# Performance work log

Hardware: AMD Instinct MI355X
Metric: run time of the kernel (lower is better)

The kernel has to match this reference:

```python
import jax, jax.numpy as jnp
import numpy as np
from jax.scipy.special import gammaln

REG = 1e-6
NHLOG2PI = -0.5 * float(np.log(2.0 * np.pi))


def _log_besseli(s, kappa):
    # Uniform asymptotic expansion (leading order) of log I_s(kappa):
    # I_s(s*x) ~ exp(s*eta) / (sqrt(2*pi*s) * (1+x^2)^(1/4))
    x = kappa / s
    sq = jnp.sqrt(1.0 + x * x)
    eta = sq + jnp.log(x) - jnp.log1p(sq)
    return s * eta - 0.5 * jnp.log(2.0 * jnp.pi * s) - 0.5 * jnp.log(sq)


def _log_C_vmf(d, kappa):
    # log C_d(kappa) = d*(-0.5 log 2pi) + s*log(kappa) - log I_s(kappa), s = d/2 - 1
    s = 0.5 * d - 1.0
    return d * NHLOG2PI + s * jnp.log(kappa) - _log_besseli(s, kappa)


def _log_surface_area(dim):
    # HypersphericalUniform.__log_surface_area
    h = (dim + 1.0) / 2.0
    return np.log(2.0) + h * np.log(np.pi) - float(jax.scipy.special.gammaln(jnp.asarray(h, jnp.float32)))


def _vmf_layer(x, w_mu, w_logk, b_mu, b_logk, in_f, out_f):
    # eval mode: weight = mu (unit-normalized flat vector), reshape(in,out).T
    mu_w = w_mu / jnp.linalg.norm(w_mu)
    mu_b = b_mu / jnp.linalg.norm(b_mu)
    W = mu_w.reshape(in_f, out_f).T  # [out, in]
    y = x @ W.T + mu_b
    kw = jnp.exp(w_logk) + REG
    kb = jnp.exp(b_logk) + REG
    d_w = float(out_f * in_f)
    d_b = float(out_f)
    # log q(w) = kappa * <mu, w> + log C_d(kappa); here w = mu so <mu,w> = 1 (computed faithfully)
    lvp = (kw * jnp.dot(mu_w, mu_w) + _log_C_vmf(d_w, kw)
           + kb * jnp.dot(mu_b, mu_b) + _log_C_vmf(d_b, kb))
    # NOTE: source bug preserved -- bias prior also uses dim = out*in
    lp = -_log_surface_area(d_w) - _log_surface_area(d_w)
    return y, lvp, lp


def _gaussian_last_layer(x, w_mu, w_rho, b_mu, b_rho):
    # eval mode: weight = mu, bias = mu
    y = x @ w_mu.T + b_mu
    sw = jnp.log1p(jnp.exp(w_rho))
    sb = jnp.log1p(jnp.exp(b_rho))
    # log q at mu: (-log sqrt(2pi) - log sigma - 0).sum()
    lvp = jnp.sum(NHLOG2PI - jnp.log(sw)) + jnp.sum(NHLOG2PI - jnp.log(sb))
    # prior: PI=1, sigma1=1 -> standard normal logpdf summed
    lp = jnp.sum(NHLOG2PI - 0.5 * w_mu ** 2) + jnp.sum(NHLOG2PI - 0.5 * b_mu ** 2)
    return y, lvp, lp


def setup_inputs() -> dict:
    key = jax.random.key(0)
    ks = jax.random.split(key, 13)
    B, IN, H, OUT = 1024, 4096, 4096, 5
    return {
        "x": jax.random.normal(ks[0], (B, IN), jnp.float32),
        "w1_mu": jax.random.normal(ks[1], (H * IN,), jnp.float32),
        "w1_logkappa": jnp.float32(2.0),
        "b1_mu": jax.random.normal(ks[2], (H,), jnp.float32),
        "b1_logkappa": jnp.float32(2.0),
        "w2_mu": jax.random.normal(ks[3], (H * H,), jnp.float32),
        "w2_logkappa": jnp.float32(2.0),
        "b2_mu": jax.random.normal(ks[4], (H,), jnp.float32),
        "b2_logkappa": jnp.float32(2.0),
        "w3_mu": jax.random.uniform(ks[5], (OUT, H), jnp.float32, -0.2, 0.2),
        "w3_rho": jax.random.uniform(ks[6], (OUT, H), jnp.float32, -5.0, -4.0),
        "b3_mu": jax.random.uniform(ks[7], (OUT,), jnp.float32, -0.2, 0.2),
        "b3_rho": jax.random.uniform(ks[8], (OUT,), jnp.float32, -5.0, -4.0),
    }


def reference(x, w1_mu, w1_logkappa, b1_mu, b1_logkappa,
              w2_mu, w2_logkappa, b2_mu, b2_logkappa,
              w3_mu, w3_rho, b3_mu, b3_rho):
    IN, H, OUT = 4096, 4096, 5
    h1, lvp1, lp1 = _vmf_layer(x, w1_mu, w1_logkappa, b1_mu, b1_logkappa, IN, H)
    h1 = jax.nn.relu(h1)
    h2, lvp2, lp2 = _vmf_layer(h1, w2_mu, w2_logkappa, b2_mu, b2_logkappa, H, H)
    h2 = jax.nn.relu(h2)
    y, lvp3, lp3 = _gaussian_last_layer(h2, w3_mu, w3_rho, b3_mu, b3_rho)
    out = jax.nn.log_softmax(y, axis=-1)
    log_var_post = lvp1 + lvp2 + lvp3
    log_prior = lp1 + lp2 + lp3
    return out, log_var_post, jnp.asarray(log_prior, out.dtype)
```

## Files before the change

### kernel.cpp

```cpp
#include <hip/hip_runtime.h>
#include <cstdint>


#define NH (-0.9189385332046727)
#define DPI 3.141592653589793238462643383279502884

typedef short s16x8 __attribute__((ext_vector_type(8)));
typedef float f32x4 __attribute__((ext_vector_type(4)));

static __device__ __forceinline__ ushort f2bf(float f) {
  uint32_t u = __float_as_uint(f);
  u += 0x7fffu + ((u >> 16) & 1u);
  return (ushort)(u >> 16);
}
static __device__ __forceinline__ float bf2f(ushort h) {
  return __uint_as_float(((uint32_t)h) << 16);
}

static __device__ __forceinline__ void gload16(const void* g, void* l) {
  __builtin_amdgcn_global_load_lds(
      (__attribute__((address_space(1))) void*)g,
      (__attribute__((address_space(3))) void*)l,
      16, 0, 0);
}

__global__ void reduce_k(const float* __restrict__ x, int n,
                         double* __restrict__ part, int mode) {
  double a = 0.0;
  const int tid = blockIdx.x * blockDim.x + threadIdx.x;
  const int stride = gridDim.x * blockDim.x;
  const int n4 = n >> 2;
  for (int i = tid; i < n4; i += stride) {
    float4 v = reinterpret_cast<const float4*>(x)[i];
    if (mode == 0) {
      a += (double)v.x * v.x + (double)v.y * v.y +
           (double)v.z * v.z + (double)v.w * v.w;
    } else {
      a += log(log1p(exp((double)v.x)));
      a += log(log1p(exp((double)v.y)));
      a += log(log1p(exp((double)v.z)));
      a += log(log1p(exp((double)v.w)));
    }
  }
  for (int i = (n4 << 2) + tid; i < n; i += stride) {
    float v = x[i];
    a += (mode == 0) ? (double)v * v : log(log1p(exp((double)v)));
  }
  for (int o = 32; o > 0; o >>= 1) a += __shfl_down(a, o);
  __shared__ double red[4];
  if ((threadIdx.x & 63) == 0) red[threadIdx.x >> 6] = a;
  __syncthreads();
  if (threadIdx.x == 0) part[blockIdx.x] = red[0] + red[1] + red[2] + red[3];
}

static __device__ double logC_vmf(double d, double kappa) {
  double s  = 0.5 * d - 1.0;
  double x  = kappa / s;
  double sq = sqrt(1.0 + x * x);
  double eta = sq + log(x) - log1p(sq);
  double lb  = s * eta - 0.5 * log(2.0 * DPI * s) - 0.5 * log(sq);
  return d * NH + s * log(kappa) - lb;
}

__global__ void finalize_k(const double* __restrict__ part,
                           const float* lkw1, const float* lkb1,
                           const float* lkw2, const float* lkb2,
                           float* __restrict__ params,
                           float* __restrict__ out_sc) {
  __shared__ double S[8];
  __shared__ double tmp[4];
  const int t = threadIdx.x;
  for (int ai = 0; ai < 8; ai++) {
    double v = part[ai * 512 + t] + part[ai * 512 + t + 256];
    for (int o = 32; o > 0; o >>= 1) v += __shfl_down(v, o);
    if ((t & 63) == 0) tmp[t >> 6] = v;
    __syncthreads();
    if (t == 0) S[ai] = tmp[0] + tmp[1] + tmp[2] + tmp[3];
    __syncthreads();
  }
  if (t == 0) {
    double Sw1 = S[0], Sb1 = S[1], Sw2 = S[2], Sb2 = S[3];
    double Sw3 = S[4], Sb3 = S[5], R6 = S[6], R7 = S[7];
    params[0] = (float)(1.0 / sqrt(Sw1));
    params[1] = (float)(1.0 / sqrt(Sb1));
    params[2] = (float)(1.0 / sqrt(Sw2));
    params[3] = (float)(1.0 / sqrt(Sb2));
    const double dw = 16777216.0, db = 4096.0;
    double kw1 = exp((double)lkw1[0]) + 1e-6;
    double kb1 = exp((double)lkb1[0]) + 1e-6;
    double kw2 = exp((double)lkw2[0]) + 1e-6;
    double kb2 = exp((double)lkb2[0]) + 1e-6;
    double lvp = kw1 + logC_vmf(dw, kw1) + kb1 + logC_vmf(db, kb1)
               + kw2 + logC_vmf(dw, kw2) + kb2 + logC_vmf(db, kb2)
               + 20485.0 * NH - R6 - R7;
    double h64 = (dw + 1.0) * 0.5;
    double hf  = (double)(float)h64;
    double lsa = log(2.0) + h64 * log(DPI) - lgamma(hf);
    double lp  = -4.0 * lsa + 20485.0 * NH - 0.5 * (Sw3 + Sb3);
    out_sc[0] = (float)lvp;
    out_sc[1] = (float)lp;
  }
}

__global__ void split_plain_k(const float* __restrict__ in,
                              ushort* __restrict__ hi, ushort* __restrict__ lo,
                              int n4) {
  int i = blockIdx.x * blockDim.x + threadIdx.x;
  if (i >= n4) return;
  float4 v = reinterpret_cast<const float4*>(in)[i];
  ushort4 h, l;
  h.x = f2bf(v.x); l.x = f2bf(v.x - bf2f(h.x));
  h.y = f2bf(v.y); l.y = f2bf(v.y - bf2f(h.y));
  h.z = f2bf(v.z); l.z = f2bf(v.z - bf2f(h.z));
  h.w = f2bf(v.w); l.w = f2bf(v.w - bf2f(h.w));
  reinterpret_cast<ushort4*>(hi)[i] = h;
  reinterpret_cast<ushort4*>(lo)[i] = l;
}

__global__ void split_transpose_k(const float* __restrict__ in,
                                  const float* __restrict__ sp,
                                  ushort* __restrict__ hi,
                                  ushort* __restrict__ lo) {
  __shared__ float tile[64][33];
  const float s = sp[0];
  const int tx = threadIdx.x, ty = threadIdx.y;
  const int n0 = blockIdx.x * 32, k0 = blockIdx.y * 64;
#pragma unroll
  for (int r = 0; r < 8; r++)
    tile[ty + r * 8][tx] = in[(size_t)(k0 + ty + r * 8) * 4096 + n0 + tx];
  __syncthreads();
#pragma unroll
  for (int r = 0; r < 4; r++) {
    const int nn = ty + r * 8;
    float v0 = tile[2 * tx][nn] * s;
    float v1 = tile[2 * tx + 1][nn] * s;
    ushort2 h, l;
    h.x = f2bf(v0); l.x = f2bf(v0 - bf2f(h.x));
    h.y = f2bf(v1); l.y = f2bf(v1 - bf2f(h.y));
    size_t o = ((size_t)(n0 + nn) * 4096 + k0 + 2 * tx) >> 1;
    reinterpret_cast<ushort2*>(hi)[o] = h;
    reinterpret_cast<ushort2*>(lo)[o] = l;
  }
}

__global__ __launch_bounds__(256) void gemm_split_k(
    const ushort* __restrict__ Ahi, const ushort* __restrict__ Alo,
    const ushort* __restrict__ Bhi, const ushort* __restrict__ Blo,
    const float* __restrict__ bias, const float* __restrict__ bsp,
    ushort* __restrict__ Ohi, ushort* __restrict__ Olo,
    float* __restrict__ Of,
    int M, int N, int K, int mode) {
  __shared__ ushort As[2][64 * 32];
  __shared__ ushort Bs[2][128 * 32];
  const int t = threadIdx.x;
  const int lane = t & 63, wid = t >> 6;
  const int wm = wid >> 1, wn = wid & 1;
  const int bm = blockIdx.y, bn = blockIdx.x;
  const int lr = lane & 15, lk = (lane >> 4) * 8;

  f32x4 acc[2][4];
#pragma unroll
  for (int i = 0; i < 2; i++)
#pragma unroll
    for (int j = 0; j < 4; j++) acc[i][j] = (f32x4){0.f, 0.f, 0.f, 0.f};

  const size_t arow = (size_t)(bm * 64) * K;
  const size_t brow = (size_t)(bn * 128) * K;
  const int ar = t >> 2, ac = (t & 3) * 8;

  for (int k0 = 0; k0 < K; k0 += 32) {
    {
      const size_t ga = arow + (size_t)ar * K + k0 + ac;
      gload16(Ahi + ga, &As[0][t * 8]);
      gload16(Alo + ga, &As[1][t * 8]);
    }
#pragma unroll
    for (int q = 0; q < 2; q++) {
      const int L = q * 256 + t;
      const size_t gb = brow + (size_t)(L >> 2) * K + k0 + (L & 3) * 8;
      gload16(Bhi + gb, &Bs[0][L * 8]);
      gload16(Blo + gb, &Bs[1][L * 8]);
    }
    __syncthreads();
    s16x8 ah[2], al[2], bh[4], bl[4];
#pragma unroll
    for (int i = 0; i < 2; i++) {
      const int ra = (wm * 32 + i * 16 + lr) * 32 + lk;
      ah[i] = *(const s16x8*)&As[0][ra];
      al[i] = *(const s16x8*)&As[1][ra];
    }
#pragma unroll
    for (int j = 0; j < 4; j++) {
      const int rb = (wn * 64 + j * 16 + lr) * 32 + lk;
      bh[j] = *(const s16x8*)&Bs[0][rb];
      bl[j] = *(const s16x8*)&Bs[1][rb];
    }
#pragma unroll
    for (int i = 0; i < 2; i++)
#pragma unroll
      for (int j = 0; j < 4; j++) {
        acc[i][j] = __builtin_amdgcn_mfma_f32_16x16x32_bf16(ah[i], bh[j], acc[i][j], 0, 0, 0);
        acc[i][j] = __builtin_amdgcn_mfma_f32_16x16x32_bf16(ah[i], bl[j], acc[i][j], 0, 0, 0);
        acc[i][j] = __builtin_amdgcn_mfma_f32_16x16x32_bf16(al[i], bh[j], acc[i][j], 0, 0, 0);
      }
    __syncthreads();
  }

  const float bsc = bsp[0];
  const int rb0 = bm * 64 + wm * 32 + (lane >> 4) * 4;
  const int cb0 = bn * 128 + wn * 64 + lr;
#pragma unroll
  for (int j = 0; j < 4; j++) {
    const int col = cb0 + j * 16;
    const float bv = bias[col] * bsc;
#pragma unroll
    for (int i = 0; i < 2; i++) {
#pragma unroll
      for (int r = 0; r < 4; r++) {
        const int row = rb0 + i * 16 + r;
        float v = fmaxf(acc[i][j][r] + bv, 0.0f);
        const size_t o = (size_t)row * N + col;
        if (mode == 0) {
          ushort h = f2bf(v);
          Ohi[o] = h;
          Olo[o] = f2bf(v - bf2f(h));
        } else {
          Of[o] = v;
        }
      }
    }
  }
}

__global__ void layer3_k(const float* __restrict__ h2,
                         const float* __restrict__ w3,
                         const float* __restrict__ b3,
                         float* __restrict__ out) {
  const int row = blockIdx.x;
  const int t = threadIdx.x;
  const float* hr = h2 + (size_t)row * 4096;
  float a[5] = {0.f, 0.f, 0.f, 0.f, 0.f};
  for (int k = t; k < 4096; k += 256) {
    const float h = hr[k];
#pragma unroll
    for (int o = 0; o < 5; o++) a[o] += h * w3[o * 4096 + k];
  }
#pragma unroll
  for (int o = 0; o < 5; o++)
    for (int s = 32; s > 0; s >>= 1) a[o] += __shfl_down(a[o], s);
  __shared__ float red[4][5];
  if ((t & 63) == 0) {
#pragma unroll
    for (int o = 0; o < 5; o++) red[t >> 6][o] = a[o];
  }
  __syncthreads();
  if (t == 0) {
    float y[5];
#pragma unroll
    for (int o = 0; o < 5; o++)
      y[o] = red[0][o] + red[1][o] + red[2][o] + red[3][o] + b3[o];
    float m = y[0];
    for (int o = 1; o < 5; o++) m = fmaxf(m, y[o]);
    float ssum = 0.f;
    for (int o = 0; o < 5; o++) ssum += expf(y[o] - m);
    const float ls = m + logf(ssum);
    for (int o = 0; o < 5; o++) out[row * 5 + o] = y[o] - ls;
  }
}

extern "C" void kernel_launch(void* const* d_in, const int* in_sizes, int n_in,
                              void* d_out, int out_size, void* d_ws, size_t ws_size,
                              hipStream_t stream) {
  const float* x     = (const float*)d_in[0];
  const float* w1mu  = (const float*)d_in[1];
  const float* lkw1  = (const float*)d_in[2];
  const float* b1mu  = (const float*)d_in[3];
  const float* lkb1  = (const float*)d_in[4];
  const float* w2mu  = (const float*)d_in[5];
  const float* lkw2  = (const float*)d_in[6];
  const float* b2mu  = (const float*)d_in[7];
  const float* lkb2  = (const float*)d_in[8];
  const float* w3mu  = (const float*)d_in[9];
  const float* w3rho = (const float*)d_in[10];
  const float* b3mu  = (const float*)d_in[11];
  const float* b3rho = (const float*)d_in[12];
  float* outp = (float*)d_out;

  char* w = (char*)d_ws;
  double* part  = (double*)w;
  float* params = (float*)(w + 32768);
  ushort* xhi  = (ushort*)(w + 65536);
  ushort* xlo  = xhi  + (size_t)1024 * 4096;
  ushort* h1hi = xlo  + (size_t)1024 * 4096;
  ushort* h1lo = h1hi + (size_t)1024 * 4096;
  ushort* wthi = (ushort*)(h1lo + (size_t)1024 * 4096);
  ushort* wtlo = wthi + (size_t)4096 * 4096;
  float*  h2   = (float*)xhi;

  reduce_k<<<512, 256, 0, stream>>>(w1mu, 16777216, part + 0 * 512, 0);
  reduce_k<<<512, 256, 0, stream>>>(b1mu, 4096,     part + 1 * 512, 0);
  reduce_k<<<512, 256, 0, stream>>>(w2mu, 16777216, part + 2 * 512, 0);
  reduce_k<<<512, 256, 0, stream>>>(b2mu, 4096,     part + 3 * 512, 0);
  reduce_k<<<512, 256, 0, stream>>>(w3mu, 20480,    part + 4 * 512, 0);
  reduce_k<<<512, 256, 0, stream>>>(b3mu, 5,        part + 5 * 512, 0);
  reduce_k<<<512, 256, 0, stream>>>(w3rho, 20480,   part + 6 * 512, 1);
  reduce_k<<<512, 256, 0, stream>>>(b3rho, 5,       part + 7 * 512, 1);
  finalize_k<<<1, 256, 0, stream>>>(part, lkw1, lkb1, lkw2, lkb2,
                                    params, outp + 5120);
  split_plain_k<<<4096, 256, 0, stream>>>(x, xhi, xlo, 1048576);
  split_transpose_k<<<dim3(128, 64), dim3(32, 8), 0, stream>>>(w1mu, params + 0, wthi, wtlo);
  gemm_split_k<<<dim3(32, 16), 256, 0, stream>>>(xhi, xlo, wthi, wtlo,
                                                 b1mu, params + 1,
                                                 h1hi, h1lo, nullptr,
                                                 1024, 4096, 4096, 0);
  split_transpose_k<<<dim3(128, 64), dim3(32, 8), 0, stream>>>(w2mu, params + 2, wthi, wtlo);
  gemm_split_k<<<dim3(32, 16), 256, 0, stream>>>(h1hi, h1lo, wthi, wtlo,
                                                 b2mu, params + 3,
                                                 nullptr, nullptr, h2,
                                                 1024, 4096, 4096, 1);
  layer3_k<<<1024, 256, 0, stream>>>(h2, w3mu, b3mu, outp);
}
```

Before: 513.3 us.

## Fuse weight norm reduction into transpose-split and double-buffer GEMM LDS

After: 568.4 us. 1.11x slower.

```diff
diff --git a/kernel.cpp b/kernel.cpp
--- a/kernel.cpp
+++ b/kernel.cpp
@@ -53,6 +53,29 @@
   if (threadIdx.x == 0) part[blockIdx.x] = red[0] + red[1] + red[2] + red[3];
 }
 
+__global__ void norms_k(const double* __restrict__ pw, int nw,
+                        const double* __restrict__ pb, int nb,
+                        float* __restrict__ out2) {
+  __shared__ double red[4];
+  const int t = threadIdx.x;
+  double s[2];
+  const double* p[2] = {pw, pb};
+  const int   cn[2] = {nw, nb};
+  for (int q = 0; q < 2; q++) {
+    double v = 0.0;
+    for (int i = t; i < cn[q]; i += 256) v += p[q][i];
+    for (int o = 32; o > 0; o >>= 1) v += __shfl_down(v, o);
+    if ((t & 63) == 0) red[t >> 6] = v;
+    __syncthreads();
+    s[q] = red[0] + red[1] + red[2] + red[3];
+    __syncthreads();
+  }
+  if (t == 0) {
+    out2[0] = (float)(1.0 / sqrt(s[0]));
+    out2[1] = (float)(1.0 / sqrt(s[1]));
+  }
+}
+
 static __device__ double logC_vmf(double d, double kappa) {
   double s  = 0.5 * d - 1.0;
   double x  = kappa / s;
@@ -62,29 +85,26 @@
   return d * NH + s * log(kappa) - lb;
 }
 
-__global__ void finalize_k(const double* __restrict__ part,
+__global__ void finalize_k(const double* __restrict__ P,
                            const float* lkw1, const float* lkb1,
                            const float* lkw2, const float* lkb2,
-                           float* __restrict__ params,
                            float* __restrict__ out_sc) {
   __shared__ double S[8];
-  __shared__ double tmp[4];
+  __shared__ double red[4];
+  const int offs[8] = {0, 16384, 8192, 16392, 16400, 16408, 16409, 16417};
+  const int cnts[8] = {8192, 8, 8192, 8, 8, 1, 8, 1};
   const int t = threadIdx.x;
   for (int ai = 0; ai < 8; ai++) {
-    double v = part[ai * 512 + t] + part[ai * 512 + t + 256];
+    double v = 0.0;
+    for (int i = t; i < cnts[ai]; i += 256) v += P[offs[ai] + i];
     for (int o = 32; o > 0; o >>= 1) v += __shfl_down(v, o);
-    if ((t & 63) == 0) tmp[t >> 6] = v;
-    __syncthreads();
-    if (t == 0) S[ai] = tmp[0] + tmp[1] + tmp[2] + tmp[3];
+    if ((t & 63) == 0) red[t >> 6] = v;
+    __syncthreads();
+    if (t == 0) S[ai] = red[0] + red[1] + red[2] + red[3];
     __syncthreads();
   }
   if (t == 0) {
-    double Sw1 = S[0], Sb1 = S[1], Sw2 = S[2], Sb2 = S[3];
     double Sw3 = S[4], Sb3 = S[5], R6 = S[6], R7 = S[7];
-    params[0] = (float)(1.0 / sqrt(Sw1));
-    params[1] = (float)(1.0 / sqrt(Sb1));
-    params[2] = (float)(1.0 / sqrt(Sw2));
-    params[3] = (float)(1.0 / sqrt(Sb2));
     const double dw = 16777216.0, db = 4096.0;
     double kw1 = exp((double)lkw1[0]) + 1e-6;
     double kb1 = exp((double)lkb1[0]) + 1e-6;
@@ -118,22 +138,26 @@
 }
 
 __global__ void split_transpose_k(const float* __restrict__ in,
-                                  const float* __restrict__ sp,
                                   ushort* __restrict__ hi,
-                                  ushort* __restrict__ lo) {
+                                  ushort* __restrict__ lo,
+                                  double* __restrict__ part) {
   __shared__ float tile[64][33];
-  const float s = sp[0];
+  __shared__ double red[4];
   const int tx = threadIdx.x, ty = threadIdx.y;
   const int n0 = blockIdx.x * 32, k0 = blockIdx.y * 64;
-#pragma unroll
-  for (int r = 0; r < 8; r++)
-    tile[ty + r * 8][tx] = in[(size_t)(k0 + ty + r * 8) * 4096 + n0 + tx];
+  double a = 0.0;
+#pragma unroll
+  for (int r = 0; r < 8; r++) {
+    float v = in[(size_t)(k0 + ty + r * 8) * 4096 + n0 + tx];
+    tile[ty + r * 8][tx] = v;
+    a += (double)v * v;
+  }
   __syncthreads();
 #pragma unroll
   for (int r = 0; r < 4; r++) {
     const int nn = ty + r * 8;
-    float v0 = tile[2 * tx][nn] * s;
-    float v1 = tile[2 * tx + 1][nn] * s;
+    float v0 = tile[2 * tx][nn];
+    float v1 = tile[2 * tx + 1][nn];
     ushort2 h, l;
     h.x = f2bf(v0); l.x = f2bf(v0 - bf2f(h.x));
     h.y = f2bf(v1); l.y = f2bf(v1 - bf2f(h.y));
@@ -141,17 +165,23 @@
     reinterpret_cast<ushort2*>(hi)[o] = h;
     reinterpret_cast<ushort2*>(lo)[o] = l;
   }
+  const int tid = ty * 32 + tx;
+  for (int o = 32; o > 0; o >>= 1) a += __shfl_down(a, o);
+  if ((tid & 63) == 0) red[tid >> 6] = a;
+  __syncthreads();
+  if (tid == 0)
+    part[blockIdx.y * gridDim.x + blockIdx.x] = red[0] + red[1] + red[2] + red[3];
 }
 
 __global__ __launch_bounds__(256) void gemm_split_k(
     const ushort* __restrict__ Ahi, const ushort* __restrict__ Alo,
     const ushort* __restrict__ Bhi, const ushort* __restrict__ Blo,
-    const float* __restrict__ bias, const float* __restrict__ bsp,
+    const float* __restrict__ bias, const float* __restrict__ scales,
     ushort* __restrict__ Ohi, ushort* __restrict__ Olo,
     float* __restrict__ Of,
     int M, int N, int K, int mode) {
-  __shared__ ushort As[2][64 * 32];
-  __shared__ ushort Bs[2][128 * 32];
+  __shared__ ushort As[2][2][64 * 32];
+  __shared__ ushort Bs[2][2][128 * 32];
   const int t = threadIdx.x;
   const int lane = t & 63, wid = t >> 6;
   const int wm = wid >> 1, wn = wid & 1;
@@ -168,32 +198,32 @@
   const size_t brow = (size_t)(bn * 128) * K;
   const int ar = t >> 2, ac = (t & 3) * 8;
 
-  for (int k0 = 0; k0 < K; k0 += 32) {
-    {
-      const size_t ga = arow + (size_t)ar * K + k0 + ac;
-      gload16(Ahi + ga, &As[0][t * 8]);
-      gload16(Alo + ga, &As[1][t * 8]);
-    }
+  auto STAGE = [&](int buf, int k0) {
+    const size_t ga = arow + (size_t)ar * K + k0 + ac;
+    gload16(Ahi + ga, &As[buf][0][t * 8]);
+    gload16(Alo + ga, &As[buf][1][t * 8]);
 #pragma unroll
     for (int q = 0; q < 2; q++) {
       const int L = q * 256 + t;
       const size_t gb = brow + (size_t)(L >> 2) * K + k0 + (L & 3) * 8;
-      gload16(Bhi + gb, &Bs[0][L * 8]);
-      gload16(Blo + gb, &Bs[1][L * 8]);
-    }
-    __syncthreads();
+      gload16(Bhi + gb, &Bs[buf][0][L * 8]);
+      gload16(Blo + gb, &Bs[buf][1][L * 8]);
+    }
+  };
+
+  auto COMPUTE = [&](int buf) {
     s16x8 ah[2], al[2], bh[4], bl[4];
 #pragma unroll
     for (int i = 0; i < 2; i++) {
       const int ra = (wm * 32 + i * 16 + lr) * 32 + lk;
-      ah[i] = *(const s16x8*)&As[0][ra];
-      al[i] = *(const s16x8*)&As[1][ra];
+      ah[i] = *(const s16x8*)&As[buf][0][ra];
+      al[i] = *(const s16x8*)&As[buf][1][ra];
     }
 #pragma unroll
     for (int j = 0; j < 4; j++) {
       const int rb = (wn * 64 + j * 16 + lr) * 32 + lk;
-      bh[j] = *(const s16x8*)&Bs[0][rb];
-      bl[j] = *(const s16x8*)&Bs[1][rb];
+      bh[j] = *(const s16x8*)&Bs[buf][0][rb];
+      bl[j] = *(const s16x8*)&Bs[buf][1][rb];
     }
 #pragma unroll
     for (int i = 0; i < 2; i++)
@@ -203,10 +233,20 @@
         acc[i][j] = __builtin_amdgcn_mfma_f32_16x16x32_bf16(ah[i], bl[j], acc[i][j], 0, 0, 0);
         acc[i][j] = __builtin_amdgcn_mfma_f32_16x16x32_bf16(al[i], bh[j], acc[i][j], 0, 0, 0);
       }
-    __syncthreads();
-  }
-
-  const float bsc = bsp[0];
+  };
+
+  STAGE(0, 0);
+  __syncthreads();
+  int cur = 0;
+  for (int k0 = 32; k0 < K; k0 += 32) {
+    STAGE(cur ^ 1, k0);
+    COMPUTE(cur);
+    __syncthreads();
+    cur ^= 1;
+  }
+  COMPUTE(cur);
+
+  const float wsc = scales[0], bsc = scales[1];
   const int rb0 = bm * 64 + wm * 32 + (lane >> 4) * 4;
   const int cb0 = bn * 128 + wn * 64 + lr;
 #pragma unroll
@@ -218,7 +258,7 @@
 #pragma unroll
       for (int r = 0; r < 4; r++) {
         const int row = rb0 + i * 16 + r;
-        float v = fmaxf(acc[i][j][r] + bv, 0.0f);
+        float v = fmaxf(fmaf(acc[i][j][r], wsc, bv), 0.0f);
         const size_t o = (size_t)row * N + col;
         if (mode == 0) {
           ushort h = f2bf(v);
@@ -287,9 +327,17 @@
   float* outp = (float*)d_out;
 
   char* w = (char*)d_ws;
-  double* part  = (double*)w;
-  float* params = (float*)(w + 32768);
-  ushort* xhi  = (ushort*)(w + 65536);
+  double* P    = (double*)w;
+  double* Pw1  = P;
+  double* Pw2  = P + 8192;
+  double* Pb1  = P + 16384;
+  double* Pb2  = P + 16392;
+  double* Pw3  = P + 16400;
+  double* Pb3  = P + 16408;
+  double* Pr3  = P + 16409;
+  double* Pbr3 = P + 16417;
+  float* params = (float*)(w + 140 * 1024);
+  ushort* xhi  = (ushort*)(w + 256 * 1024);
   ushort* xlo  = xhi  + (size_t)1024 * 4096;
   ushort* h1hi = xlo  + (size_t)1024 * 4096;
   ushort* h1lo = h1hi + (size_t)1024 * 4096;
@@ -297,26 +345,25 @@
   ushort* wtlo = wthi + (size_t)4096 * 4096;
   float*  h2   = (float*)xhi;
 
-  reduce_k<<<512, 256, 0, stream>>>(w1mu, 16777216, part + 0 * 512, 0);
-  reduce_k<<<512, 256, 0, stream>>>(b1mu, 4096,     part + 1 * 512, 0);
-  reduce_k<<<512, 256, 0, stream>>>(w2mu, 16777216, part + 2 * 512, 0);
-  reduce_k<<<512, 256, 0, stream>>>(b2mu, 4096,     part + 3 * 512, 0);
-  reduce_k<<<512, 256, 0, stream>>>(w3mu, 20480,    part + 4 * 512, 0);
-  reduce_k<<<512, 256, 0, stream>>>(b3mu, 5,        part + 5 * 512, 0);
-  reduce_k<<<512, 256, 0, stream>>>(w3rho, 20480,   part + 6 * 512, 1);
-  reduce_k<<<512, 256, 0, stream>>>(b3rho, 5,       part + 7 * 512, 1);
-  finalize_k<<<1, 256, 0, stream>>>(part, lkw1, lkb1, lkw2, lkb2,
-                                    params, outp + 5120);
   split_plain_k<<<4096, 256, 0, stream>>>(x, xhi, xlo, 1048576);
-  split_transpose_k<<<dim3(128, 64), dim3(32, 8), 0, stream>>>(w1mu, params + 0, wthi, wtlo);
+  split_transpose_k<<<dim3(128, 64), dim3(32, 8), 0, stream>>>(w1mu, wthi, wtlo, Pw1);
+  reduce_k<<<8, 256, 0, stream>>>(b1mu, 4096, Pb1, 0);
+  reduce_k<<<8, 256, 0, stream>>>(w3mu, 20480, Pw3, 0);
+  reduce_k<<<1, 256, 0, stream>>>(b3mu, 5, Pb3, 0);
+  reduce_k<<<8, 256, 0, stream>>>(w3rho, 20480, Pr3, 1);
+  reduce_k<<<1, 256, 0, stream>>>(b3rho, 5, Pbr3, 1);
+  norms_k<<<1, 256, 0, stream>>>(Pw1, 8192, Pb1, 8, params + 0);
   gemm_split_k<<<dim3(32, 16), 256, 0, stream>>>(xhi, xlo, wthi, wtlo,
-                                                 b1mu, params + 1,
+                                                 b1mu, params + 0,
                                                  h1hi, h1lo, nullptr,
                                                  1024, 4096, 4096, 0);
-  split_transpose_k<<<dim3(128, 64), dim3(32, 8), 0, stream>>>(w2mu, params + 2, wthi, wtlo);
+  split_transpose_k<<<dim3(128, 64), dim3(32, 8), 0, stream>>>(w2mu, wthi, wtlo, Pw2);
+  reduce_k<<<8, 256, 0, stream>>>(b2mu, 4096, Pb2, 0);
+  norms_k<<<1, 256, 0, stream>>>(Pw2, 8192, Pb2, 8, params + 2);
   gemm_split_k<<<dim3(32, 16), 256, 0, stream>>>(h1hi, h1lo, wthi, wtlo,
-                                                 b2mu, params + 3,
+                                                 b2mu, params + 2,
                                                  nullptr, nullptr, h2,
                                                  1024, 4096, 4096, 1);
+  finalize_k<<<1, 256, 0, stream>>>(P, lkw1, lkb1, lkw2, lkb2, outp + 5120);
   layer3_k<<<1024, 256, 0, stream>>>(h2, w3mu, b3mu, outp);
 }
```
